# Optimization experiments

Hardware: AMD Instinct MI355X
Metric: run time of the kernel (lower is better)

## Reference

```python
import jax, jax.numpy as jnp
import numpy as np

N_NODES = 50000
N_EDGES = 1600000
EMB = 8  # graph_embedding_size


def setup_inputs() -> dict:
    key = jax.random.key(0)
    ks = jax.random.split(key, 16)
    def lin(k, fan_in, fan_out):
        b = 1.0 / np.sqrt(fan_in)
        kw, kb = jax.random.split(k)
        W = jax.random.uniform(kw, (fan_in, fan_out), jnp.float32, -b, b)
        bias = jax.random.uniform(kb, (fan_out,), jnp.float32, -b, b)
        return W, bias
    Wm1, bm1 = lin(ks[0], 2 + EMB, 32)   # mlp_m layer 1 (in: x_j(9) ++ edge_attr(1))
    Wm2, bm2 = lin(ks[1], 32, 32)        # mlp_m layer 2
    Wu1, bu1 = lin(ks[2], 33 + EMB, 16)  # mlp_U layer 1 (in: x(9) ++ aggr(32))
    Wu2, bu2 = lin(ks[3], 16, EMB)       # mlp_U layer 2
    Wh1, bh1 = lin(ks[4], EMB, 16)       # h2o MLP
    Wh2, bh2 = lin(ks[5], 16, 1)         # h2o final Linear + Sigmoid
    x = jax.random.normal(ks[6], (N_NODES, 1 + EMB), jnp.float32)
    edge_index = jax.random.randint(ks[7], (2, N_EDGES), 0, N_NODES, jnp.int64)
    edge_attr = jax.random.normal(ks[8], (N_EDGES, 1), jnp.float32)
    return {"x": x, "edge_index": edge_index, "edge_attr": edge_attr,
            "Wm1": Wm1, "bm1": bm1, "Wm2": Wm2, "bm2": bm2,
            "Wu1": Wu1, "bu1": bu1, "Wu2": Wu2, "bu2": bu2,
            "Wh1": Wh1, "bh1": bh1, "Wh2": Wh2, "bh2": bh2}


def _conv(x, src, dst, edge_attr, Wm1, bm1, Wm2, bm2, Wu1, bu1, Wu2, bu2):
    # message: mlp_m(cat[x_j, edge_attr])  (x_j gathered from source nodes)
    m = jnp.concatenate([x[src], edge_attr], axis=1)        # [E, 10]
    m = jax.nn.relu(m @ Wm1 + bm1)
    m = jax.nn.relu(m @ Wm2 + bm2)                          # [E, 32]
    # aggregate: scatter-sum to destination nodes
    aggr = jax.ops.segment_sum(m, dst, num_segments=x.shape[0])  # [N, 32]
    # update: keep state channel, recompute embedding
    h = jnp.concatenate([x, aggr], axis=1)                  # [N, 41]
    h = jax.nn.relu(h @ Wu1 + bu1)
    h = jax.nn.relu(h @ Wu2 + bu2)                          # [N, 8]
    return jnp.concatenate([x[:, :1], h], axis=1)           # [N, 9]


def reference(x, edge_index, edge_attr, Wm1, bm1, Wm2, bm2, Wu1, bu1, Wu2, bu2,
              Wh1, bh1, Wh2, bh2):
    src, dst = edge_index[0], edge_index[1]
    h = x
    for _ in range(3):  # fixed 3 message-passing rounds, shared weights
        h = _conv(h, src, dst, edge_attr, Wm1, bm1, Wm2, bm2, Wu1, bu1, Wu2, bu2)
    # h2o on the embedding part
    o = jax.nn.relu(h[:, 1:] @ Wh1 + bh1)
    return jax.nn.sigmoid(o @ Wh2 + bh2)                    # [N, 1]
```

## Files before the change

kernel.cpp:

```cpp
#include <hip/hip_runtime.h>
#include <hip/hip_bf16.h>
#include <math.h>

typedef float f8 __attribute__((ext_vector_type(8)));
typedef short short8 __attribute__((ext_vector_type(8)));
typedef float f4v __attribute__((ext_vector_type(4)));

__device__ __forceinline__ unsigned int bfpack(float lo, float hi) {
  union { __hip_bfloat16 h; unsigned short u; } a, b;
  a.h = __float2bfloat16(lo);
  b.h = __float2bfloat16(hi);
  return (unsigned int)a.u | ((unsigned int)b.u << 16);
}


#define NB1 256
#define NBKT 1024

__global__ __launch_bounds__(256) void chist_kernel(const int* __restrict__ ei,
    int* __restrict__ ghist, int E, int epb) {
  __shared__ int h[NBKT];
  #pragma unroll
  for (int i = 0; i < NBKT / 256; ++i) h[threadIdx.x + i * 256] = 0;
  __syncthreads();
  int b = blockIdx.x;
  int s = b * epb, epos = min(E, s + epb);
  for (int e = s + threadIdx.x; e < epos; e += 256)
    atomicAdd(&h[((unsigned)ei[E + e]) >> 6], 1);
  __syncthreads();
  #pragma unroll
  for (int i = 0; i < NBKT / 256; ++i) {
    int k = threadIdx.x + i * 256;
    ghist[k * NB1 + b] = h[k];
  }
}

__global__ __launch_bounds__(256) void bscan_kernel(int* __restrict__ data,
    int* __restrict__ bsum, int n) {
  __shared__ int sh[256];
  int i = blockIdx.x * 256 + threadIdx.x;
  int v = (i < n) ? data[i] : 0;
  sh[threadIdx.x] = v;
  __syncthreads();
  #pragma unroll
  for (int off = 1; off < 256; off <<= 1) {
    int u = (threadIdx.x >= off) ? sh[threadIdx.x - off] : 0;
    __syncthreads();
    sh[threadIdx.x] += u;
    __syncthreads();
  }
  if (i < n) data[i] = sh[threadIdx.x] - v;
  if (threadIdx.x == 255) bsum[blockIdx.x] = sh[255];
}

__global__ __launch_bounds__(1024) void midscan_kernel(int* __restrict__ bsum, int nb) {
  __shared__ int sh[1024];
  int v = (threadIdx.x < nb) ? bsum[threadIdx.x] : 0;
  sh[threadIdx.x] = v;
  __syncthreads();
  #pragma unroll
  for (int off = 1; off < 1024; off <<= 1) {
    int u = (threadIdx.x >= off) ? sh[threadIdx.x - off] : 0;
    __syncthreads();
    sh[threadIdx.x] += u;
    __syncthreads();
  }
  if (threadIdx.x < nb) bsum[threadIdx.x] = sh[threadIdx.x] - v;
}

__global__ __launch_bounds__(256) void badd_kernel(int* __restrict__ data,
    const int* __restrict__ bsum, int n) {
  int i = blockIdx.x * 256 + threadIdx.x;
  if (i < n) data[i] += bsum[blockIdx.x];
}

__global__ __launch_bounds__(256) void cscatter_kernel(const int* __restrict__ ei,
    const float* __restrict__ ea, const int* __restrict__ ghist,
    int2* __restrict__ tmp, int E, int epb) {
  __shared__ int cur[NBKT];
  int b = blockIdx.x;
  #pragma unroll
  for (int i = 0; i < NBKT / 256; ++i) {
    int k = threadIdx.x + i * 256;
    cur[k] = ghist[k * NB1 + b];
  }
  __syncthreads();
  int s = b * epb, epos = min(E, s + epb);
  for (int e = s + threadIdx.x; e < epos; e += 256) {
    int src = ei[e];
    int d   = ei[E + e];
    float v = ea[e];
    int pos = atomicAdd(&cur[((unsigned)d) >> 6], 1);
    tmp[pos] = make_int2(src | (d << 16), __float_as_int(v));
  }
}

__global__ __launch_bounds__(256) void fsort_kernel(const int2* __restrict__ tmp,
    const int* __restrict__ ghist, int2* __restrict__ sedge, int E) {
  __shared__ int h[64], cur[64];
  int k = blockIdx.x;
  int s = ghist[k * NB1];
  int epos = (k == NBKT - 1) ? E : ghist[(k + 1) * NB1];
  if (threadIdx.x < 64) h[threadIdx.x] = 0;
  __syncthreads();
  for (int e = s + threadIdx.x; e < epos; e += 256)
    atomicAdd(&h[(((unsigned)tmp[e].x) >> 16) & 63], 1);
  __syncthreads();
  if (threadIdx.x == 0) {
    int run = s;
    #pragma unroll
    for (int f = 0; f < 64; ++f) { cur[f] = run; run += h[f]; }
  }
  __syncthreads();
  for (int e = s + threadIdx.x; e < epos; e += 256) {
    int2 t = tmp[e];
    int pos = atomicAdd(&cur[(((unsigned)t.x) >> 16) & 63], 1);
    sedge[pos] = t;
  }
}


__global__ __launch_bounds__(256) void premsg_kernel(const float* __restrict__ h,
    const float* __restrict__ Wm1, const float* __restrict__ bm1,
    float* __restrict__ P, int N) {
  int n = blockIdx.x * blockDim.x + threadIdx.x;
  if (n >= N) return;
  float hv[9];
  #pragma unroll
  for (int i = 0; i < 9; ++i) hv[i] = h[(size_t)n * 9 + i];
  float acc[32];
  #pragma unroll
  for (int k = 0; k < 32; ++k) acc[k] = bm1[k];
  #pragma unroll
  for (int i = 0; i < 9; ++i)
    #pragma unroll
    for (int k = 0; k < 32; ++k) acc[k] = fmaf(hv[i], Wm1[i * 32 + k], acc[k]);
  float4* Pv = (float4*)(P + (size_t)n * 32);
  #pragma unroll
  for (int jv = 0; jv < 8; ++jv)
    Pv[jv] = make_float4(acc[jv * 4], acc[jv * 4 + 1], acc[jv * 4 + 2], acc[jv * 4 + 3]);
}


__global__ __launch_bounds__(256) void agg_kernel(
    const int2* __restrict__ sedge, const float* __restrict__ Pin,
    float* __restrict__ G, const float* __restrict__ Wm1,
    const float* __restrict__ Wm2, const float* __restrict__ bm2, int E) {
  __shared__ uint4 Abuf[4][4][64];
  __shared__ float Msg[4][64][33];
  __shared__ int   Dst[256];

  const int tid = threadIdx.x;
  const int w = tid >> 6, l = tid & 63;
  const int e = blockIdx.x * 256 + tid;

  int2 se = (e < E) ? sedge[e] : make_int2((int)0xFFFF0000u, 0);
  int dst = ((unsigned)se.x) >> 16;
  int src = se.x & 0xFFFF;
  Dst[tid] = dst;
  float eav = __int_as_float(se.y);
  const f8* __restrict__ Pv  = (const f8*)(Pin + (size_t)src * 32);
  const f8* __restrict__ W1t = (const f8*)(Wm1 + 288);
  const int mt = l >> 4, r = l & 15;
  #pragma unroll
  for (int q = 0; q < 4; ++q) {
    f8 pv = Pv[q];
    f8 wq = W1t[q];
    f8 hv;
    #pragma unroll
    for (int k = 0; k < 8; ++k) hv[k] = fmaxf(fmaf(eav, wq[k], pv[k]), 0.f);
    uint4 ck;
    ck.x = bfpack(hv[0], hv[1]);
    ck.y = bfpack(hv[2], hv[3]);
    ck.z = bfpack(hv[4], hv[5]);
    ck.w = bfpack(hv[6], hv[7]);
    Abuf[w][mt][r + 16 * q] = ck;
  }

  const int col0 = l & 15;
  const int k0 = (l >> 4) * 8;
  uint4 bhi[2], blo[2];
  #pragma unroll
  for (int nt = 0; nt < 2; ++nt) {
    unsigned int hi[8], lo[8];
    #pragma unroll
    for (int j = 0; j < 8; ++j) {
      float wv = Wm2[(k0 + j) * 32 + nt * 16 + col0];
      union { __hip_bfloat16 h; unsigned short u; } c;
      c.h = __float2bfloat16(wv);
      hi[j] = c.u;
      float wh = __bfloat162float(c.h);
      c.h = __float2bfloat16(wv - wh);
      lo[j] = c.u;
    }
    bhi[nt] = make_uint4(hi[0] | (hi[1] << 16), hi[2] | (hi[3] << 16),
                         hi[4] | (hi[5] << 16), hi[6] | (hi[7] << 16));
    blo[nt] = make_uint4(lo[0] | (lo[1] << 16), lo[2] | (lo[3] << 16),
                         lo[4] | (lo[5] << 16), lo[6] | (lo[7] << 16));
  }
  f4v acc[4][2];
  #pragma unroll
  for (int nt = 0; nt < 2; ++nt) {
    float bias = bm2[nt * 16 + col0];
    #pragma unroll
    for (int m = 0; m < 4; ++m) {
      acc[m][nt][0] = bias; acc[m][nt][1] = bias;
      acc[m][nt][2] = bias; acc[m][nt][3] = bias;
    }
  }
  #pragma unroll
  for (int m = 0; m < 4; ++m) {
    uint4 av = Abuf[w][m][l];
    short8 a8 = __builtin_bit_cast(short8, av);
    #pragma unroll
    for (int nt = 0; nt < 2; ++nt) {
      acc[m][nt] = __builtin_amdgcn_mfma_f32_16x16x32_bf16(
          a8, __builtin_bit_cast(short8, blo[nt]), acc[m][nt], 0, 0, 0);
      acc[m][nt] = __builtin_amdgcn_mfma_f32_16x16x32_bf16(
          a8, __builtin_bit_cast(short8, bhi[nt]), acc[m][nt], 0, 0, 0);
    }
  }
  const int rq = (l >> 4) * 4;
  #pragma unroll
  for (int m = 0; m < 4; ++m)
    #pragma unroll
    for (int nt = 0; nt < 2; ++nt)
      #pragma unroll
      for (int i = 0; i < 4; ++i)
        Msg[w][m * 16 + rq + i][nt * 16 + col0] = fmaxf(acc[m][nt][i], 0.f);

  const int c = tid & 31;
  const int g = tid >> 5;
  const int w2 = g >> 1;
  const int base = (g & 1) * 32;
  float rsum = 0.f;
  #pragma unroll 4
  for (int i = 0; i < 32; ++i) {
    int idx = base + i;
    int d = Dst[w2 * 64 + idx];
    rsum += Msg[w2][idx][c];
    int dn = (i == 31) ? -2 : Dst[w2 * 64 + idx + 1];
    if (d != dn) {
      if (d != 0xFFFF) atomicAdd(&G[(size_t)d * 32 + c], rsum);
      rsum = 0.f;
    }
  }
}


template <int MODE>
__global__ __launch_bounds__(256) void update_kernel(
    const float* __restrict__ G, const float* __restrict__ hin,
    float* __restrict__ hout, float* __restrict__ Pout,
    const float* __restrict__ Wm1, const float* __restrict__ bm1,
    const float* __restrict__ Wu1, const float* __restrict__ bu1,
    const float* __restrict__ Wu2, const float* __restrict__ bu2,
    const float* __restrict__ Wh1, const float* __restrict__ bh1,
    const float* __restrict__ Wh2, const float* __restrict__ bh2,
    float* __restrict__ out, int N) {
  int n = blockIdx.x * blockDim.x + threadIdx.x;
  if (n >= N) return;
  float aggr[32];
  const float4* Gv = (const float4*)(G + (size_t)n * 32);
  #pragma unroll
  for (int jv = 0; jv < 8; ++jv) {
    float4 v = Gv[jv];
    aggr[jv*4+0] = v.x; aggr[jv*4+1] = v.y; aggr[jv*4+2] = v.z; aggr[jv*4+3] = v.w;
  }
  float hv[9];
  #pragma unroll
  for (int i = 0; i < 9; ++i) hv[i] = hin[(size_t)n * 9 + i];
  float u1[16];
  #pragma unroll
  for (int q = 0; q < 16; ++q) {
    float a = bu1[q];
    #pragma unroll
    for (int i = 0; i < 9; ++i) a = fmaf(hv[i], Wu1[i * 16 + q], a);
    #pragma unroll
    for (int k = 0; k < 32; ++k) a = fmaf(aggr[k], Wu1[(9 + k) * 16 + q], a);
    u1[q] = fmaxf(a, 0.f);
  }
  float emb[8];
  #pragma unroll
  for (int r = 0; r < 8; ++r) {
    float a = bu2[r];
    #pragma unroll
    for (int q = 0; q < 16; ++q) a = fmaf(u1[q], Wu2[q * 8 + r], a);
    emb[r] = fmaxf(a, 0.f);
  }
  if constexpr (MODE == 0) {
    float acc[32];
    #pragma unroll
    for (int k = 0; k < 32; ++k) acc[k] = fmaf(hv[0], Wm1[k], bm1[k]);
    #pragma unroll
    for (int r = 0; r < 8; ++r)
      #pragma unroll
      for (int k = 0; k < 32; ++k) acc[k] = fmaf(emb[r], Wm1[(1 + r) * 32 + k], acc[k]);
    hout[(size_t)n * 9] = hv[0];
    #pragma unroll
    for (int r = 0; r < 8; ++r) hout[(size_t)n * 9 + 1 + r] = emb[r];
    float4* Pv = (float4*)(Pout + (size_t)n * 32);
    #pragma unroll
    for (int jv = 0; jv < 8; ++jv)
      Pv[jv] = make_float4(acc[jv*4], acc[jv*4+1], acc[jv*4+2], acc[jv*4+3]);
  } else {
    float o[16];
    #pragma unroll
    for (int q = 0; q < 16; ++q) {
      float a = bh1[q];
      #pragma unroll
      for (int r = 0; r < 8; ++r) a = fmaf(emb[r], Wh1[r * 16 + q], a);
      o[q] = fmaxf(a, 0.f);
    }
    float z = bh2[0];
    #pragma unroll
    for (int q = 0; q < 16; ++q) z = fmaf(o[q], Wh2[q], z);
    out[n] = 1.f / (1.f + expf(-z));
  }
}


extern "C" void kernel_launch(void* const* d_in, const int* in_sizes, int n_in,
                              void* d_out, int out_size, void* d_ws, size_t ws_size,
                              hipStream_t stream) {
  const float* x   = (const float*)d_in[0];
  const int*   ei  = (const int*)d_in[1];
  const float* ea  = (const float*)d_in[2];
  const float* Wm1 = (const float*)d_in[3];
  const float* bm1 = (const float*)d_in[4];
  const float* Wm2 = (const float*)d_in[5];
  const float* bm2 = (const float*)d_in[6];
  const float* Wu1 = (const float*)d_in[7];
  const float* bu1 = (const float*)d_in[8];
  const float* Wu2 = (const float*)d_in[9];
  const float* bu2 = (const float*)d_in[10];
  const float* Wh1 = (const float*)d_in[11];
  const float* bh1 = (const float*)d_in[12];
  const float* Wh2 = (const float*)d_in[13];
  const float* bh2 = (const float*)d_in[14];
  float* out = (float*)d_out;
  const int N = in_sizes[0] / 9;
  const int E = in_sizes[2];

  char* wsb = (char*)d_ws;
  size_t pos = 0;
  auto alloc = [&](size_t b) {
    pos = (pos + 255) & ~(size_t)255;
    char* p = wsb + pos;
    pos += b;
    return (void*)p;
  };
  int*   ghist = (int*)alloc((size_t)NBKT * NB1 * 4);
  int*   bsum  = (int*)alloc(1024 * 4);
  int2*  tmp   = (int2*)alloc((size_t)E * 8);
  int2*  sedge = (int2*)alloc((size_t)E * 8);
  float* P0    = (float*)alloc((size_t)N * 32 * 4);
  float* P1    = (float*)alloc((size_t)N * 32 * 4);
  float* G     = (float*)alloc((size_t)N * 32 * 4);
  float* hA    = (float*)alloc((size_t)N * 9 * 4);
  float* hB    = (float*)alloc((size_t)N * 9 * 4);

  const int epb = (E + NB1 - 1) / NB1;
  const int ng  = NBKT * NB1;
  const int nsb = ng / 256;

  premsg_kernel<<<(N + 255) / 256, 256, 0, stream>>>(x, Wm1, bm1, P0, N);
  chist_kernel<<<NB1, 256, 0, stream>>>(ei, ghist, E, epb);
  bscan_kernel<<<nsb, 256, 0, stream>>>(ghist, bsum, ng);
  midscan_kernel<<<1, 1024, 0, stream>>>(bsum, nsb);
  badd_kernel<<<nsb, 256, 0, stream>>>(ghist, bsum, ng);
  cscatter_kernel<<<NB1, 256, 0, stream>>>(ei, ea, ghist, tmp, E, epb);
  fsort_kernel<<<NBKT, 256, 0, stream>>>(tmp, ghist, sedge, E);

  int ab = (E + 255) / 256;
  int ub = (N + 255) / 256;
  hipMemsetAsync(G, 0, (size_t)N * 32 * 4, stream);
  agg_kernel<<<ab, 256, 0, stream>>>(sedge, P0, G, Wm1, Wm2, bm2, E);
  update_kernel<0><<<ub, 256, 0, stream>>>(G, x, hA, P1,
      Wm1, bm1, Wu1, bu1, Wu2, bu2, Wh1, bh1, Wh2, bh2, nullptr, N);
  hipMemsetAsync(G, 0, (size_t)N * 32 * 4, stream);
  agg_kernel<<<ab, 256, 0, stream>>>(sedge, P1, G, Wm1, Wm2, bm2, E);
  update_kernel<0><<<ub, 256, 0, stream>>>(G, hA, hB, P0,
      Wm1, bm1, Wu1, bu1, Wu2, bu2, Wh1, bh1, Wh2, bh2, nullptr, N);
  hipMemsetAsync(G, 0, (size_t)N * 32 * 4, stream);
  agg_kernel<<<ab, 256, 0, stream>>>(sedge, P0, G, Wm1, Wm2, bm2, E);
  update_kernel<1><<<ub, 256, 0, stream>>>(G, hB, nullptr, nullptr,
      Wm1, bm1, Wu1, bu1, Wu2, bu2, Wh1, bh1, Wh2, bh2, out, N);
}
```

Before: 339.1 us.

## Make agg_kernel persistent with grid-stride tiles and prefetch of the next tile's gathers

The aggregation kernel now launches a fixed grid of 768 blocks that loop over 256-edge tiles, rather than one block per tile. Each iteration loads the next tile's sorted edge record and gathered P row before processing the current tile, so the gather latency overlaps with the MFMA and atomic work. The per-block Wm2 hi/lo bf16 split and the bias loads are done once per block instead of once per tile. The trade-offs are fewer resident waves per CU to hide latency and higher register pressure from the double-buffered P rows.

```diff
diff --git a/kernel.cpp b/kernel.cpp
--- a/kernel.cpp
+++ b/kernel.cpp
@@ -145,40 +145,24 @@
 __global__ __launch_bounds__(256) void agg_kernel(
     const int2* __restrict__ sedge, const float* __restrict__ Pin,
     float* __restrict__ G, const float* __restrict__ Wm1,
-    const float* __restrict__ Wm2, const float* __restrict__ bm2, int E) {
+    const float* __restrict__ Wm2, const float* __restrict__ bm2,
+    int E, int ntiles, int nblk) {
   __shared__ uint4 Abuf[4][4][64];
   __shared__ float Msg[4][64][33];
   __shared__ int   Dst[256];
 
   const int tid = threadIdx.x;
   const int w = tid >> 6, l = tid & 63;
-  const int e = blockIdx.x * 256 + tid;
-
-  int2 se = (e < E) ? sedge[e] : make_int2((int)0xFFFF0000u, 0);
-  int dst = ((unsigned)se.x) >> 16;
-  int src = se.x & 0xFFFF;
-  Dst[tid] = dst;
-  float eav = __int_as_float(se.y);
-  const f8* __restrict__ Pv  = (const f8*)(Pin + (size_t)src * 32);
-  const f8* __restrict__ W1t = (const f8*)(Wm1 + 288);
   const int mt = l >> 4, r = l & 15;
-  #pragma unroll
-  for (int q = 0; q < 4; ++q) {
-    f8 pv = Pv[q];
-    f8 wq = W1t[q];
-    f8 hv;
-    #pragma unroll
-    for (int k = 0; k < 8; ++k) hv[k] = fmaxf(fmaf(eav, wq[k], pv[k]), 0.f);
-    uint4 ck;
-    ck.x = bfpack(hv[0], hv[1]);
-    ck.y = bfpack(hv[2], hv[3]);
-    ck.z = bfpack(hv[4], hv[5]);
-    ck.w = bfpack(hv[6], hv[7]);
-    Abuf[w][mt][r + 16 * q] = ck;
-  }
-
   const int col0 = l & 15;
   const int k0 = (l >> 4) * 8;
+  const int rq = (l >> 4) * 4;
+  const int c = tid & 31;
+  const int g = tid >> 5;
+  const int w2 = g >> 1;
+  const int base = (g & 1) * 32;
+  const f8* __restrict__ W1t = (const f8*)(Wm1 + 288);
+
   uint4 bhi[2], blo[2];
   #pragma unroll
   for (int nt = 0; nt < 2; ++nt) {
@@ -186,64 +170,105 @@
     #pragma unroll
     for (int j = 0; j < 8; ++j) {
       float wv = Wm2[(k0 + j) * 32 + nt * 16 + col0];
-      union { __hip_bfloat16 h; unsigned short u; } c;
-      c.h = __float2bfloat16(wv);
-      hi[j] = c.u;
-      float wh = __bfloat162float(c.h);
-      c.h = __float2bfloat16(wv - wh);
-      lo[j] = c.u;
+      union { __hip_bfloat16 h; unsigned short u; } cv;
+      cv.h = __float2bfloat16(wv);
+      hi[j] = cv.u;
+      float wh = __bfloat162float(cv.h);
+      cv.h = __float2bfloat16(wv - wh);
+      lo[j] = cv.u;
     }
     bhi[nt] = make_uint4(hi[0] | (hi[1] << 16), hi[2] | (hi[3] << 16),
                          hi[4] | (hi[5] << 16), hi[6] | (hi[7] << 16));
     blo[nt] = make_uint4(lo[0] | (lo[1] << 16), lo[2] | (lo[3] << 16),
                          lo[4] | (lo[5] << 16), lo[6] | (lo[7] << 16));
   }
-  f4v acc[4][2];
-  #pragma unroll
-  for (int nt = 0; nt < 2; ++nt) {
-    float bias = bm2[nt * 16 + col0];
+  float bias[2] = {bm2[col0], bm2[16 + col0]};
+
+  int t = blockIdx.x;
+  if (t >= ntiles) return;
+  int e = t * 256 + tid;
+  int2 se = (e < E) ? sedge[e] : make_int2((int)0xFFFF0000u, 0);
+  f8 p[4];
+  {
+    const f8* Pv = (const f8*)(Pin + (size_t)(se.x & 0xFFFF) * 32);
+    #pragma unroll
+    for (int q = 0; q < 4; ++q) p[q] = Pv[q];
+  }
+
+  while (true) {
+    int tn = t + nblk;
+    bool more = tn < ntiles;
+    int en = more ? tn * 256 + tid : e;
+    int2 sen = (en < E) ? sedge[en] : make_int2((int)0xFFFF0000u, 0);
+    f8 pn[4];
+    {
+      const f8* Pv = (const f8*)(Pin + (size_t)(sen.x & 0xFFFF) * 32);
+      #pragma unroll
+      for (int q = 0; q < 4; ++q) pn[q] = Pv[q];
+    }
+
+    int dst = ((unsigned)se.x) >> 16;
+    Dst[tid] = dst;
+    float eav = __int_as_float(se.y);
+    #pragma unroll
+    for (int q = 0; q < 4; ++q) {
+      f8 wq = W1t[q];
+      f8 hv;
+      #pragma unroll
+      for (int k = 0; k < 8; ++k) hv[k] = fmaxf(fmaf(eav, wq[k], p[q][k]), 0.f);
+      uint4 ck;
+      ck.x = bfpack(hv[0], hv[1]);
+      ck.y = bfpack(hv[2], hv[3]);
+      ck.z = bfpack(hv[4], hv[5]);
+      ck.w = bfpack(hv[6], hv[7]);
+      Abuf[w][mt][r + 16 * q] = ck;
+    }
+
+    f4v acc[4][2];
+    #pragma unroll
+    for (int nt = 0; nt < 2; ++nt)
+      #pragma unroll
+      for (int m = 0; m < 4; ++m) {
+        acc[m][nt][0] = bias[nt]; acc[m][nt][1] = bias[nt];
+        acc[m][nt][2] = bias[nt]; acc[m][nt][3] = bias[nt];
+      }
     #pragma unroll
     for (int m = 0; m < 4; ++m) {
-      acc[m][nt][0] = bias; acc[m][nt][1] = bias;
-      acc[m][nt][2] = bias; acc[m][nt][3] = bias;
-    }
-  }
-  #pragma unroll
-  for (int m = 0; m < 4; ++m) {
-    uint4 av = Abuf[w][m][l];
-    short8 a8 = __builtin_bit_cast(short8, av);
-    #pragma unroll
-    for (int nt = 0; nt < 2; ++nt) {
-      acc[m][nt] = __builtin_amdgcn_mfma_f32_16x16x32_bf16(
-          a8, __builtin_bit_cast(short8, blo[nt]), acc[m][nt], 0, 0, 0);
-      acc[m][nt] = __builtin_amdgcn_mfma_f32_16x16x32_bf16(
-          a8, __builtin_bit_cast(short8, bhi[nt]), acc[m][nt], 0, 0, 0);
-    }
-  }
-  const int rq = (l >> 4) * 4;
-  #pragma unroll
-  for (int m = 0; m < 4; ++m)
-    #pragma unroll
-    for (int nt = 0; nt < 2; ++nt)
-      #pragma unroll
-      for (int i = 0; i < 4; ++i)
-        Msg[w][m * 16 + rq + i][nt * 16 + col0] = fmaxf(acc[m][nt][i], 0.f);
-
-  const int c = tid & 31;
-  const int g = tid >> 5;
-  const int w2 = g >> 1;
-  const int base = (g & 1) * 32;
-  float rsum = 0.f;
-  #pragma unroll 4
-  for (int i = 0; i < 32; ++i) {
-    int idx = base + i;
-    int d = Dst[w2 * 64 + idx];
-    rsum += Msg[w2][idx][c];
-    int dn = (i == 31) ? -2 : Dst[w2 * 64 + idx + 1];
-    if (d != dn) {
-      if (d != 0xFFFF) atomicAdd(&G[(size_t)d * 32 + c], rsum);
-      rsum = 0.f;
-    }
+      uint4 av = Abuf[w][m][l];
+      short8 a8 = __builtin_bit_cast(short8, av);
+      #pragma unroll
+      for (int nt = 0; nt < 2; ++nt) {
+        acc[m][nt] = __builtin_amdgcn_mfma_f32_16x16x32_bf16(
+            a8, __builtin_bit_cast(short8, blo[nt]), acc[m][nt], 0, 0, 0);
+        acc[m][nt] = __builtin_amdgcn_mfma_f32_16x16x32_bf16(
+            a8, __builtin_bit_cast(short8, bhi[nt]), acc[m][nt], 0, 0, 0);
+      }
+    }
+    #pragma unroll
+    for (int m = 0; m < 4; ++m)
+      #pragma unroll
+      for (int nt = 0; nt < 2; ++nt)
+        #pragma unroll
+        for (int i = 0; i < 4; ++i)
+          Msg[w][m * 16 + rq + i][nt * 16 + col0] = fmaxf(acc[m][nt][i], 0.f);
+
+    float rsum = 0.f;
+    #pragma unroll 4
+    for (int i = 0; i < 32; ++i) {
+      int idx = base + i;
+      int d = Dst[w2 * 64 + idx];
+      rsum += Msg[w2][idx][c];
+      int dn = (i == 31) ? -2 : Dst[w2 * 64 + idx + 1];
+      if (d != dn) {
+        if (d != 0xFFFF) atomicAdd(&G[(size_t)d * 32 + c], rsum);
+        rsum = 0.f;
+      }
+    }
+
+    if (!more) break;
+    t = tn; e = en; se = sen;
+    #pragma unroll
+    for (int q = 0; q < 4; ++q) p[q] = pn[q];
   }
 }
 
@@ -372,18 +397,20 @@
   cscatter_kernel<<<NB1, 256, 0, stream>>>(ei, ea, ghist, tmp, E, epb);
   fsort_kernel<<<NBKT, 256, 0, stream>>>(tmp, ghist, sedge, E);
 
-  int ab = (E + 255) / 256;
+  const int ntiles = (E + 255) / 256;
+  const int nblk = 768;
+  int ab = (ntiles < nblk) ? ntiles : nblk;
   int ub = (N + 255) / 256;
   hipMemsetAsync(G, 0, (size_t)N * 32 * 4, stream);
-  agg_kernel<<<ab, 256, 0, stream>>>(sedge, P0, G, Wm1, Wm2, bm2, E);
+  agg_kernel<<<ab, 256, 0, stream>>>(sedge, P0, G, Wm1, Wm2, bm2, E, ntiles, nblk);
   update_kernel<0><<<ub, 256, 0, stream>>>(G, x, hA, P1,
       Wm1, bm1, Wu1, bu1, Wu2, bu2, Wh1, bh1, Wh2, bh2, nullptr, N);
   hipMemsetAsync(G, 0, (size_t)N * 32 * 4, stream);
-  agg_kernel<<<ab, 256, 0, stream>>>(sedge, P1, G, Wm1, Wm2, bm2, E);
+  agg_kernel<<<ab, 256, 0, stream>>>(sedge, P1, G, Wm1, Wm2, bm2, E, ntiles, nblk);
   update_kernel<0><<<ub, 256, 0, stream>>>(G, hA, hB, P0,
       Wm1, bm1, Wu1, bu1, Wu2, bu2, Wh1, bh1, Wh2, bh2, nullptr, N);
   hipMemsetAsync(G, 0, (size_t)N * 32 * 4, stream);
-  agg_kernel<<<ab, 256, 0, stream>>>(sedge, P0, G, Wm1, Wm2, bm2, E);
+  agg_kernel<<<ab, 256, 0, stream>>>(sedge, P0, G, Wm1, Wm2, bm2, E, ntiles, nblk);
   update_kernel<1><<<ub, 256, 0, stream>>>(G, hB, nullptr, nullptr,
       Wm1, bm1, Wu1, bu1, Wu2, bu2, Wh1, bh1, Wh2, bh2, out, N);
 }
```

Result: faster. 310.1 us (-8.6%).
